# Optimization experiments

Measured on AMD Instinct MI355X. Metric: run time of the kernel, lower is better.

## Reference

```python
import jax, jax.numpy as jnp
import numpy as np
from jax import lax

EPS = 1e-5

# ---- 1-bit activation quantizer with straight-through estimator ----
@jax.custom_vjp
def ste_sign(x):
    return jnp.sign(x)

def _ste_sign_fwd(x):
    return jnp.sign(x), x

def _ste_sign_bwd(res, g):
    x = res
    # clipped STE: pass gradient where |x| <= 1
    return (g * (jnp.abs(x) <= 1.0).astype(g.dtype),)

ste_sign.defvjp(_ste_sign_fwd, _ste_sign_bwd)

# ---- 1-bit weight binarization: sign(w) * per-out-channel mean(|w|), STE ----
@jax.custom_vjp
def bin_weight(w):
    alpha = jnp.mean(jnp.abs(w), axis=(1, 2, 3), keepdims=True)  # [O,1,1,1]
    return jnp.sign(w) * alpha

def _bw_fwd(w):
    return bin_weight(w), w

def _bw_bwd(res, g):
    w = res
    # weight_clip=1: straight-through inside the clip range
    return (g * (jnp.abs(w) <= 1.0).astype(g.dtype),)

bin_weight.defvjp(_bw_fwd, _bw_bwd)

def conv3x3(x, w):
    # zero padding=1, stride=1, NCHW / OIHW
    return lax.conv_general_dilated(
        x, w, window_strides=(1, 1), padding=((1, 1), (1, 1)),
        dimension_numbers=('NCHW', 'OIHW', 'NCHW'))

def batchnorm(x, gamma, beta):
    # training-mode BN with batch statistics over (N,H,W)
    mean = jnp.mean(x, axis=(0, 2, 3), keepdims=True)
    var = jnp.var(x, axis=(0, 2, 3), keepdims=True)
    xn = (x - mean) * lax.rsqrt(var + EPS)
    return xn * gamma[None, :, None, None] + beta[None, :, None, None]


def setup_inputs() -> dict:
    key = jax.random.key(0)
    k1, k2, k3 = jax.random.split(key, 3)
    N, C, H, W = 32, 256, 56, 56
    return {
        'x': jax.random.normal(k1, (N, C, H, W), dtype=jnp.float32),
        'w1': jax.random.normal(k2, (C, C, 3, 3), dtype=jnp.float32) * 0.05,
        'gamma1': jnp.ones((C,), dtype=jnp.float32),
        'beta1': jnp.zeros((C,), dtype=jnp.float32),
        'w2': jax.random.normal(k3, (C, C, 3, 3), dtype=jnp.float32) * 0.05,
        'gamma2': jnp.ones((C,), dtype=jnp.float32),
        'beta2': jnp.zeros((C,), dtype=jnp.float32),
    }


def reference(x, w1, gamma1, beta1, w2, gamma2, beta2):
    identity = x
    out = ste_sign(x)                       # quantized activation (1-bit, signed)
    out = conv3x3(out, bin_weight(w1))      # BinConv 3x3, stride 1
    out = batchnorm(out, gamma1, beta1)
    out = ste_sign(out)
    out = conv3x3(out, bin_weight(w2))
    out = batchnorm(out, gamma2, beta2)
    return out + identity                   # residual add (downsample=None)
```

## Files before the change

### kernel.cpp

```cpp
#include <hip/hip_runtime.h>
#include <stdint.h>

#define NB 32
#define CH 256
#define HH 56
#define WW 56
#define HWSZ (HH*WW)
#define NPIX (NB*HWSZ)
#define HP 58
#define WP 58
#define PADPIX (NB*HP*WP)
#define NTAPS 9
#define KKE (CH*NTAPS)
#define NPIXD 100352.0
#define WQ_CONV (NTAPS*8*8*64*16)
#define HSTRIDE 272

typedef int int4v  __attribute__((ext_vector_type(4)));
typedef int int16v __attribute__((ext_vector_type(16)));

__global__ void init_kernel(long long* __restrict__ sums8) {
    int t = blockIdx.x*256 + threadIdx.x;
    if (t < 2*8*512) sums8[t] = 0;
}

__global__ void wqpack_kernel(const float* __restrict__ w1, const float* __restrict__ w2,
                              int8_t* __restrict__ wq) {
    int t = blockIdx.x*256 + threadIdx.x;
    int conv = blockIdx.y;
    const float* w = conv ? w2 : w1;
    int lane = t & 63;
    int g = t >> 6;
    int nb = g & 7, h = g >> 3;
    int ks = h & 7, tap = h >> 3;
    int o = nb*32 + (lane & 31);
    int cin0 = ks*32 + (lane >> 5)*16;
    int wd[4];
    #pragma unroll
    for (int q = 0; q < 4; ++q) {
        int wv = 0;
        #pragma unroll
        for (int j = 0; j < 4; ++j) {
            float v = w[(size_t)(o*CH + cin0 + q*4 + j)*NTAPS + tap];
            int s = (v > 0.f) ? 1 : ((v < 0.f) ? -1 : 0);
            wv |= (s & 0xff) << (8*j);
        }
        wd[q] = wv;
    }
    *(int4v*)(wq + (size_t)conv*WQ_CONV + (size_t)t*16) = (int4v){wd[0], wd[1], wd[2], wd[3]};
}

__global__ void alpha_kernel(const float* __restrict__ w1, const float* __restrict__ w2,
                             float* __restrict__ alpha) {
    int o = blockIdx.x; int conv = blockIdx.y;
    const float* w = conv ? w2 : w1;
    float s = 0.f;
    for (int i = threadIdx.x; i < KKE; i += 256) s += fabsf(w[(size_t)o*KKE + i]);
    for (int off = 32; off; off >>= 1) s += __shfl_down(s, off);
    __shared__ float l[4];
    int lane = threadIdx.x & 63, wv = threadIdx.x >> 6;
    if (lane == 0) l[wv] = s;
    __syncthreads();
    if (threadIdx.x == 0) alpha[conv*CH + o] = (l[0]+l[1]+l[2]+l[3]) * (1.f/KKE);
}

__global__ void pack_x_kernel(const float* __restrict__ x, int8_t* __restrict__ apad) {
    int p = blockIdx.x*256 + threadIdx.x;
    if (p >= PADPIX) return;
    int n  = p / (HP*WP);
    int r  = p - n*(HP*WP);
    int hp = r / WP, wp = r - hp*WP;
    int4v* dst = (int4v*)(apad + (size_t)p*CH);
    if (hp >= 1 && hp <= HH && wp >= 1 && wp <= WW) {
        const float* xb = x + (size_t)n*CH*HWSZ + (hp-1)*WW + (wp-1);
        #pragma unroll 2
        for (int c16 = 0; c16 < 16; ++c16) {
            int wd[4];
            #pragma unroll
            for (int q = 0; q < 4; ++q) {
                int wv = 0;
                #pragma unroll
                for (int j = 0; j < 4; ++j) {
                    float v = xb[(size_t)(c16*16 + q*4 + j)*HWSZ];
                    int s = (v > 0.f) ? 1 : ((v < 0.f) ? -1 : 0);
                    wv |= (s & 0xff) << (8*j);
                }
                wd[q] = wv;
            }
            dst[c16] = (int4v){wd[0], wd[1], wd[2], wd[3]};
        }
    } else {
        int4v z = {0,0,0,0};
        #pragma unroll
        for (int c16 = 0; c16 < 16; ++c16) dst[c16] = z;
    }
}

__global__ void pack_s_kernel(const int16_t* __restrict__ cnt,
                              const float* __restrict__ ab,
                              int8_t* __restrict__ apad) {
    int p = blockIdx.x*256 + threadIdx.x;
    if (p >= PADPIX) return;
    int n  = p / (HP*WP);
    int r  = p - n*(HP*WP);
    int hp = r / WP, wp = r - hp*WP;
    int4v* dst = (int4v*)(apad + (size_t)p*CH);
    if (hp >= 1 && hp <= HH && wp >= 1 && wp <= WW) {
        const int4v* cb = (const int4v*)(cnt + ((size_t)n*HWSZ + (hp-1)*WW + (wp-1))*CH);
        #pragma unroll 2
        for (int c16 = 0; c16 < 16; ++c16) {
            int4v u0 = cb[c16*2], u1 = cb[c16*2+1];
            int wd[4];
            #pragma unroll
            for (int q = 0; q < 4; ++q) {
                int wv = 0;
                #pragma unroll
                for (int j = 0; j < 4; ++j) {
                    int e = q*4 + j;
                    int word = (e < 8) ? u0[e >> 1] : u1[(e-8) >> 1];
                    int sval = (e & 1) ? (word >> 16) : ((word << 16) >> 16);
                    int ch = c16*16 + e;
                    float v = fmaf(ab[ch], (float)sval, ab[CH + ch]);
                    int s = (v > 0.f) ? 1 : ((v < 0.f) ? -1 : 0);
                    wv |= (s & 0xff) << (8*j);
                }
                wd[q] = wv;
            }
            dst[c16] = (int4v){wd[0], wd[1], wd[2], wd[3]};
        }
    } else {
        int4v z = {0,0,0,0};
        #pragma unroll
        for (int c16 = 0; c16 < 16; ++c16) dst[c16] = z;
    }
}

#define AOFF(IT) (((((IT)>>3)/3)*10 + (((IT)>>3)%3))*HSTRIDE + ((IT)&7)*32)

__global__ __launch_bounds__(256, 2) void conv_kernel(
        const int8_t* __restrict__ apad, const int8_t* __restrict__ wq,
        int16_t* __restrict__ cnt, long long* __restrict__ sums8) {
    __shared__ __attribute__((aligned(16))) int8_t halo[200*HSTRIDE];
    int b = blockIdx.x;
    int tile = b % 49, npair = b / 49;
    int ty = tile / 7, tx = tile % 7;
    int n0 = npair * 2;
    int t = threadIdx.x;

    #pragma unroll 1
    for (int j = 0; j < 13; ++j) {
        int idx = t + j*256;
        if (idx < 3200) {
            int pix = idx >> 4, c16 = idx & 15;
            int img = (pix >= 100) ? 1 : 0;
            int hp = pix - img*100;
            int dr = hp / 10, dc = hp - dr*10;
            const int4v* src = (const int4v*)(apad +
                ((size_t)(((n0+img)*HP + ty*8+dr)*WP + tx*8+dc))*CH + c16*16);
            *(int4v*)&halo[pix*HSTRIDE + c16*16] = *src;
        }
    }
    __syncthreads();

    int lane = t & 63;
    int wv = __builtin_amdgcn_readfirstlane(t >> 6);
    int kh = lane >> 5, lr = lane & 31;
    int r0 = lr >> 3, c0 = lr & 7;
    int base0 = (r0*10 + c0)*HSTRIDE + kh*16;
    int base1 = base0 + 40*HSTRIDE;
    int base2 = base0 + 100*HSTRIDE;
    int base3 = base0 + 140*HSTRIDE;

    const int8_t* wp0 = wq + wv*2048 + lane*16;
    const int8_t* wp1 = wp0 + 1024;

    int16v acc00, acc01, acc10, acc11, acc20, acc21, acc30, acc31;
    #pragma unroll
    for (int i = 0; i < 16; ++i) {
        acc00[i]=0; acc01[i]=0; acc10[i]=0; acc11[i]=0;
        acc20[i]=0; acc21[i]=0; acc30[i]=0; acc31[i]=0;
    }

    int4v a[2][4], bb[2][2];
    a[0][0] = *(const int4v*)&halo[base0 + AOFF(0)];
    a[0][1] = *(const int4v*)&halo[base1 + AOFF(0)];
    a[0][2] = *(const int4v*)&halo[base2 + AOFF(0)];
    a[0][3] = *(const int4v*)&halo[base3 + AOFF(0)];
    bb[0][0] = *(const int4v*)(wp0);
    bb[0][1] = *(const int4v*)(wp1);

    #pragma unroll
    for (int it = 0; it < 72; ++it) {
        int cur = it & 1, nxt = cur ^ 1;
        if (it + 1 < 72) {
            a[nxt][0] = *(const int4v*)&halo[base0 + AOFF(it+1)];
            a[nxt][1] = *(const int4v*)&halo[base1 + AOFF(it+1)];
            a[nxt][2] = *(const int4v*)&halo[base2 + AOFF(it+1)];
            a[nxt][3] = *(const int4v*)&halo[base3 + AOFF(it+1)];
            bb[nxt][0] = *(const int4v*)(wp0 + (it+1)*8192);
            bb[nxt][1] = *(const int4v*)(wp1 + (it+1)*8192);
        }
        acc00 = __builtin_amdgcn_mfma_i32_32x32x32_i8(a[cur][0], bb[cur][0], acc00, 0,0,0);
        acc01 = __builtin_amdgcn_mfma_i32_32x32x32_i8(a[cur][0], bb[cur][1], acc01, 0,0,0);
        acc10 = __builtin_amdgcn_mfma_i32_32x32x32_i8(a[cur][1], bb[cur][0], acc10, 0,0,0);
        acc11 = __builtin_amdgcn_mfma_i32_32x32x32_i8(a[cur][1], bb[cur][1], acc11, 0,0,0);
        acc20 = __builtin_amdgcn_mfma_i32_32x32x32_i8(a[cur][2], bb[cur][0], acc20, 0,0,0);
        acc21 = __builtin_amdgcn_mfma_i32_32x32x32_i8(a[cur][2], bb[cur][1], acc21, 0,0,0);
        acc30 = __builtin_amdgcn_mfma_i32_32x32x32_i8(a[cur][3], bb[cur][0], acc30, 0,0,0);
        acc31 = __builtin_amdgcn_mfma_i32_32x32x32_i8(a[cur][3], bb[cur][1], acc31, 0,0,0);
    }

#define STOREACC(ACC, M, J) do { \
        int ch_ = (wv*2 + (J))*32 + lr; \
        int img_ = (M) >> 1; \
        _Pragma("unroll") \
        for (int reg = 0; reg < 16; ++reg) { \
            int row_ = (reg & 3) + 8*(reg >> 2) + 4*kh; \
            int pm_ = ((M) & 1)*32 + row_; \
            int rr_ = pm_ >> 3, cc_ = pm_ & 7; \
            cnt[(size_t)(((n0+img_)*HH + ty*8 + rr_)*WW + tx*8 + cc_)*CH + ch_] = (int16_t)ACC[reg]; \
        } \
    } while (0)

    STOREACC(acc00, 0, 0); STOREACC(acc01, 0, 1);
    STOREACC(acc10, 1, 0); STOREACC(acc11, 1, 1);
    STOREACC(acc20, 2, 0); STOREACC(acc21, 2, 1);
    STOREACC(acc30, 3, 0); STOREACC(acc31, 3, 1);
#undef STOREACC

    int s1a = 0, s2a = 0, s1b = 0, s2b = 0;
    #pragma unroll
    for (int reg = 0; reg < 16; ++reg) {
        int v;
        v = acc00[reg]; s1a += v; s2a += v*v;
        v = acc10[reg]; s1a += v; s2a += v*v;
        v = acc20[reg]; s1a += v; s2a += v*v;
        v = acc30[reg]; s1a += v; s2a += v*v;
        v = acc01[reg]; s1b += v; s2b += v*v;
        v = acc11[reg]; s1b += v; s2b += v*v;
        v = acc21[reg]; s1b += v; s2b += v*v;
        v = acc31[reg]; s1b += v; s2b += v*v;
    }
    s1a += __shfl_down(s1a, 32); s2a += __shfl_down(s2a, 32);
    s1b += __shfl_down(s1b, 32); s2b += __shfl_down(s2b, 32);
    if (lane < 32) {
        long long* sp = sums8 + (size_t)(b & 7)*512;
        int ch0 = wv*64 + lr, ch1 = ch0 + 32;
        atomicAdd((unsigned long long*)&sp[2*ch0],   (unsigned long long)(long long)s1a);
        atomicAdd((unsigned long long*)&sp[2*ch0+1], (unsigned long long)(long long)s2a);
        atomicAdd((unsigned long long*)&sp[2*ch1],   (unsigned long long)(long long)s1b);
        atomicAdd((unsigned long long*)&sp[2*ch1+1], (unsigned long long)(long long)s2b);
    }
}

__global__ void bncoef_kernel(const long long* __restrict__ sums8,
                              const float* __restrict__ alpha,
                              const float* __restrict__ gamma, const float* __restrict__ beta,
                              float* __restrict__ ab) {
    int o = threadIdx.x;
    long long S1i = 0, S2i = 0;
    #pragma unroll
    for (int k = 0; k < 8; ++k) {
        S1i += sums8[(size_t)k*512 + 2*o];
        S2i += sums8[(size_t)k*512 + 2*o + 1];
    }
    double S1 = (double)S1i, S2 = (double)S2i;
    double mean = S1 / NPIXD;
    double var  = S2 / NPIXD - mean*mean;
    double al   = (double)alpha[o];
    double rs   = 1.0 / sqrt(al*al*var + 1e-5);
    double a    = (double)gamma[o] * al * rs;
    ab[o]      = (float)a;
    ab[CH + o] = (float)((double)beta[o] - a*mean);
}

__global__ __launch_bounds__(256) void final_kernel(const int16_t* __restrict__ cnt,
        const float* __restrict__ x, const float* __restrict__ ab, float* __restrict__ out) {
    __shared__ int4v lsd4[64*32];
    int8_t* lb = (int8_t*)lsd4;
    int b = blockIdx.x;
    int n = b / 49, tile = b - n*49;
    int p0 = tile * 64;
    int t = threadIdx.x;
    const int4v* src = (const int4v*)(cnt + ((size_t)n*HWSZ + p0)*CH);
    #pragma unroll
    for (int j = 0; j < 8; ++j) {
        int c = t + j*256;
        int pix = c >> 5, c16 = c & 31;
        *(int4v*)&lb[pix*512 + ((c16*16) ^ ((pix & 15) << 4))] = src[c];
    }
    __syncthreads();
    int pixL = t & 63;
    int cb = (t >> 6) * 64;
    #pragma unroll 1
    for (int i = 0; i < 8; ++i) {
        int ch0 = cb + i*8;
        int4v v = *(const int4v*)&lb[pixL*512 + ((ch0*2) ^ ((pixL & 15) << 4))];
        #pragma unroll
        for (int j = 0; j < 8; ++j) {
            int ch = ch0 + j;
            int word = v[j >> 1];
            int sval = (j & 1) ? (word >> 16) : ((word << 16) >> 16);
            size_t g = (size_t)(n*CH + ch)*HWSZ + p0 + pixL;
            out[g] = fmaf(ab[ch], (float)sval, ab[CH + ch]) + x[g];
        }
    }
}

extern "C" void kernel_launch(void* const* d_in, const int* in_sizes, int n_in,
                              void* d_out, int out_size, void* d_ws, size_t ws_size,
                              hipStream_t stream) {
    const float* x  = (const float*)d_in[0];
    const float* w1 = (const float*)d_in[1];
    const float* g1 = (const float*)d_in[2];
    const float* b1 = (const float*)d_in[3];
    const float* w2 = (const float*)d_in[4];
    const float* g2 = (const float*)d_in[5];
    const float* b2 = (const float*)d_in[6];
    float* out = (float*)d_out;

    char* ws = (char*)d_ws;
    size_t off = 0;
    auto alloc = [&](size_t nbytes) { char* pp = ws + off; off = (off + nbytes + 255) & ~(size_t)255; return pp; };
    int8_t*   apad  = (int8_t*)alloc((size_t)PADPIX*CH);
    int16_t*  cnt   = (int16_t*)alloc((size_t)NPIX*CH*2);
    int8_t*   wq    = (int8_t*)alloc((size_t)2*WQ_CONV);
    float*    alpha = (float*)alloc((size_t)2*CH*4);
    long long* sums8 = (long long*)alloc((size_t)2*8*512*8);
    float*    ab    = (float*)alloc((size_t)2*2*CH*4);

    init_kernel<<<32, 256, 0, stream>>>(sums8);
    wqpack_kernel<<<dim3(144, 2), 256, 0, stream>>>(w1, w2, wq);
    alpha_kernel<<<dim3(CH, 2), 256, 0, stream>>>(w1, w2, alpha);
    pack_x_kernel<<<(PADPIX + 255)/256, 256, 0, stream>>>(x, apad);

    conv_kernel<<<784, 256, 0, stream>>>(apad, wq, cnt, sums8);
    bncoef_kernel<<<1, CH, 0, stream>>>(sums8, alpha, g1, b1, ab);

    pack_s_kernel<<<(PADPIX + 255)/256, 256, 0, stream>>>(cnt, ab, apad);
    conv_kernel<<<784, 256, 0, stream>>>(apad, wq + WQ_CONV, cnt, sums8 + 8*512);
    bncoef_kernel<<<1, CH, 0, stream>>>(sums8 + 8*512, alpha + CH, g2, b2, ab + 2*CH);

    final_kernel<<<1568, 256, 0, stream>>>(cnt, x, ab + 2*CH, out);
}
```

Baseline: 262.7 us.

## Split conv work across 8 waves per block, halving accumulators per wave

The conv kernel now runs 512 threads per block. Each of the 8 waves handles one image and a 64-channel slice, using 4 accumulator tiles instead of 8. The explicit double-buffered prefetch of A/B operands is dropped in favour of direct loads each iteration. The aim is fewer VGPRs per wave and more waves resident for latency hiding. The cost is that each weight fragment is now loaded twice, once per image wave, and memory latency hiding depends on the compiler and occupancy instead of software prefetch.

```diff
diff --git a/kernel.cpp b/kernel.cpp
--- a/kernel.cpp
+++ b/kernel.cpp
@@ -137,7 +137,7 @@
 
 #define AOFF(IT) (((((IT)>>3)/3)*10 + (((IT)>>3)%3))*HSTRIDE + ((IT)&7)*32)
 
-__global__ __launch_bounds__(256, 2) void conv_kernel(
+__global__ __launch_bounds__(512, 4) void conv_kernel(
         const int8_t* __restrict__ apad, const int8_t* __restrict__ wq,
         int16_t* __restrict__ cnt, long long* __restrict__ sums8) {
     __shared__ __attribute__((aligned(16))) int8_t halo[200*HSTRIDE];
@@ -148,8 +148,8 @@
     int t = threadIdx.x;
 
     #pragma unroll 1
-    for (int j = 0; j < 13; ++j) {
-        int idx = t + j*256;
+    for (int j = 0; j < 7; ++j) {
+        int idx = t + j*512;
         if (idx < 3200) {
             int pix = idx >> 4, c16 = idx & 15;
             int img = (pix >= 100) ? 1 : 0;
@@ -163,69 +163,46 @@
     __syncthreads();
 
     int lane = t & 63;
-    int wv = __builtin_amdgcn_readfirstlane(t >> 6);
+    int wvid = __builtin_amdgcn_readfirstlane(t >> 6);
+    int img  = wvid >> 2;
+    int nbp  = wvid & 3;
     int kh = lane >> 5, lr = lane & 31;
     int r0 = lr >> 3, c0 = lr & 7;
-    int base0 = (r0*10 + c0)*HSTRIDE + kh*16;
+    int base0 = (r0*10 + c0)*HSTRIDE + kh*16 + img*100*HSTRIDE;
     int base1 = base0 + 40*HSTRIDE;
-    int base2 = base0 + 100*HSTRIDE;
-    int base3 = base0 + 140*HSTRIDE;
-
-    const int8_t* wp0 = wq + wv*2048 + lane*16;
+
+    const int8_t* wp0 = wq + nbp*2048 + lane*16;
     const int8_t* wp1 = wp0 + 1024;
 
-    int16v acc00, acc01, acc10, acc11, acc20, acc21, acc30, acc31;
-    #pragma unroll
-    for (int i = 0; i < 16; ++i) {
-        acc00[i]=0; acc01[i]=0; acc10[i]=0; acc11[i]=0;
-        acc20[i]=0; acc21[i]=0; acc30[i]=0; acc31[i]=0;
-    }
-
-    int4v a[2][4], bb[2][2];
-    a[0][0] = *(const int4v*)&halo[base0 + AOFF(0)];
-    a[0][1] = *(const int4v*)&halo[base1 + AOFF(0)];
-    a[0][2] = *(const int4v*)&halo[base2 + AOFF(0)];
-    a[0][3] = *(const int4v*)&halo[base3 + AOFF(0)];
-    bb[0][0] = *(const int4v*)(wp0);
-    bb[0][1] = *(const int4v*)(wp1);
+    int16v acc00, acc01, acc10, acc11;
+    #pragma unroll
+    for (int i = 0; i < 16; ++i) { acc00[i]=0; acc01[i]=0; acc10[i]=0; acc11[i]=0; }
 
     #pragma unroll
     for (int it = 0; it < 72; ++it) {
-        int cur = it & 1, nxt = cur ^ 1;
-        if (it + 1 < 72) {
-            a[nxt][0] = *(const int4v*)&halo[base0 + AOFF(it+1)];
-            a[nxt][1] = *(const int4v*)&halo[base1 + AOFF(it+1)];
-            a[nxt][2] = *(const int4v*)&halo[base2 + AOFF(it+1)];
-            a[nxt][3] = *(const int4v*)&halo[base3 + AOFF(it+1)];
-            bb[nxt][0] = *(const int4v*)(wp0 + (it+1)*8192);
-            bb[nxt][1] = *(const int4v*)(wp1 + (it+1)*8192);
-        }
-        acc00 = __builtin_amdgcn_mfma_i32_32x32x32_i8(a[cur][0], bb[cur][0], acc00, 0,0,0);
-        acc01 = __builtin_amdgcn_mfma_i32_32x32x32_i8(a[cur][0], bb[cur][1], acc01, 0,0,0);
-        acc10 = __builtin_amdgcn_mfma_i32_32x32x32_i8(a[cur][1], bb[cur][0], acc10, 0,0,0);
-        acc11 = __builtin_amdgcn_mfma_i32_32x32x32_i8(a[cur][1], bb[cur][1], acc11, 0,0,0);
-        acc20 = __builtin_amdgcn_mfma_i32_32x32x32_i8(a[cur][2], bb[cur][0], acc20, 0,0,0);
-        acc21 = __builtin_amdgcn_mfma_i32_32x32x32_i8(a[cur][2], bb[cur][1], acc21, 0,0,0);
-        acc30 = __builtin_amdgcn_mfma_i32_32x32x32_i8(a[cur][3], bb[cur][0], acc30, 0,0,0);
-        acc31 = __builtin_amdgcn_mfma_i32_32x32x32_i8(a[cur][3], bb[cur][1], acc31, 0,0,0);
+        int4v a0 = *(const int4v*)&halo[base0 + AOFF(it)];
+        int4v a1 = *(const int4v*)&halo[base1 + AOFF(it)];
+        int4v b0 = *(const int4v*)(wp0 + it*8192);
+        int4v b1 = *(const int4v*)(wp1 + it*8192);
+        acc00 = __builtin_amdgcn_mfma_i32_32x32x32_i8(a0, b0, acc00, 0,0,0);
+        acc01 = __builtin_amdgcn_mfma_i32_32x32x32_i8(a0, b1, acc01, 0,0,0);
+        acc10 = __builtin_amdgcn_mfma_i32_32x32x32_i8(a1, b0, acc10, 0,0,0);
+        acc11 = __builtin_amdgcn_mfma_i32_32x32x32_i8(a1, b1, acc11, 0,0,0);
     }
 
 #define STOREACC(ACC, M, J) do { \
-        int ch_ = (wv*2 + (J))*32 + lr; \
-        int img_ = (M) >> 1; \
+        int ch_ = (nbp*2 + (J))*32 + lr; \
         _Pragma("unroll") \
         for (int reg = 0; reg < 16; ++reg) { \
             int row_ = (reg & 3) + 8*(reg >> 2) + 4*kh; \
-            int pm_ = ((M) & 1)*32 + row_; \
+            int pm_ = (M)*32 + row_; \
             int rr_ = pm_ >> 3, cc_ = pm_ & 7; \
-            cnt[(size_t)(((n0+img_)*HH + ty*8 + rr_)*WW + tx*8 + cc_)*CH + ch_] = (int16_t)ACC[reg]; \
+            cnt[(size_t)(((n0+img)*HH + ty*8 + rr_)*WW + tx*8 + cc_)*CH + ch_] = (int16_t)ACC[reg]; \
         } \
     } while (0)
 
     STOREACC(acc00, 0, 0); STOREACC(acc01, 0, 1);
     STOREACC(acc10, 1, 0); STOREACC(acc11, 1, 1);
-    STOREACC(acc20, 2, 0); STOREACC(acc21, 2, 1);
-    STOREACC(acc30, 3, 0); STOREACC(acc31, 3, 1);
 #undef STOREACC
 
     int s1a = 0, s2a = 0, s1b = 0, s2b = 0;
@@ -234,18 +211,14 @@
         int v;
         v = acc00[reg]; s1a += v; s2a += v*v;
         v = acc10[reg]; s1a += v; s2a += v*v;
-        v = acc20[reg]; s1a += v; s2a += v*v;
-        v = acc30[reg]; s1a += v; s2a += v*v;
         v = acc01[reg]; s1b += v; s2b += v*v;
         v = acc11[reg]; s1b += v; s2b += v*v;
-        v = acc21[reg]; s1b += v; s2b += v*v;
-        v = acc31[reg]; s1b += v; s2b += v*v;
     }
     s1a += __shfl_down(s1a, 32); s2a += __shfl_down(s2a, 32);
     s1b += __shfl_down(s1b, 32); s2b += __shfl_down(s2b, 32);
     if (lane < 32) {
         long long* sp = sums8 + (size_t)(b & 7)*512;
-        int ch0 = wv*64 + lr, ch1 = ch0 + 32;
+        int ch0 = nbp*64 + lr, ch1 = ch0 + 32;
         atomicAdd((unsigned long long*)&sp[2*ch0],   (unsigned long long)(long long)s1a);
         atomicAdd((unsigned long long*)&sp[2*ch0+1], (unsigned long long)(long long)s2a);
         atomicAdd((unsigned long long*)&sp[2*ch1],   (unsigned long long)(long long)s1b);
@@ -334,11 +307,11 @@
     alpha_kernel<<<dim3(CH, 2), 256, 0, stream>>>(w1, w2, alpha);
     pack_x_kernel<<<(PADPIX + 255)/256, 256, 0, stream>>>(x, apad);
 
-    conv_kernel<<<784, 256, 0, stream>>>(apad, wq, cnt, sums8);
+    conv_kernel<<<784, 512, 0, stream>>>(apad, wq, cnt, sums8);
     bncoef_kernel<<<1, CH, 0, stream>>>(sums8, alpha, g1, b1, ab);
 
     pack_s_kernel<<<(PADPIX + 255)/256, 256, 0, stream>>>(cnt, ab, apad);
-    conv_kernel<<<784, 256, 0, stream>>>(apad, wq + WQ_CONV, cnt, sums8 + 8*512);
+    conv_kernel<<<784, 512, 0, stream>>>(apad, wq + WQ_CONV, cnt, sums8 + 8*512);
     bncoef_kernel<<<1, CH, 0, stream>>>(sums8 + 8*512, alpha + CH, g2, b2, ab + 2*CH);
 
     final_kernel<<<1568, 256, 0, stream>>>(cnt, x, ab + 2*CH, out);
```

New measurement: 270.0 us. 2.8% more time.
